# Performance work log

Hardware: AMD Instinct MI355X
Metric: run time of the kernel (lower is better)

Reference implementation:

```python
import jax, jax.numpy as jnp
import numpy as np

V, E, H, L, B, T = 8192, 64, 256, 2, 4, 512


def setup_inputs() -> dict:
    key = jax.random.key(0)
    ks = jax.random.split(key, 20)
    s = 0.02
    emb = (jax.random.normal(ks[0], (V, E)) * s).at[0].set(0.0)  # padding_idx=0
    x = jax.random.randint(ks[1], (B, T), 0, V)
    return {
        "x": x,
        "emb": emb,
        "W_ih0": jax.random.normal(ks[2], (H, E)) * s,
        "W_hh0": jax.random.normal(ks[3], (H, H)) * s,
        "b_ih0": jnp.zeros((H,), jnp.float32),
        "b_hh0": jnp.zeros((H,), jnp.float32),
        "W_ih1": jax.random.normal(ks[4], (H, H)) * s,
        "W_hh1": jax.random.normal(ks[5], (H, H)) * s,
        "b_ih1": jnp.zeros((H,), jnp.float32),
        "b_hh1": jnp.zeros((H,), jnp.float32),
        "Wq": jax.random.normal(ks[6], (H, H)) * s,
        "Wk": jax.random.normal(ks[7], (H, H)) * s,
        "v": jax.random.normal(ks[8], (H,)) * s,
        "gamma": jnp.ones((2 * H,), jnp.float32),
        "beta": jnp.zeros((2 * H,), jnp.float32),
        "Wfc": jax.random.normal(ks[9], (V, 2 * H)) * s,
        "bfc": jnp.zeros((V,), jnp.float32),
    }


def _rnn_layer(xs, W_ih, W_hh, b_ih, b_hh):
    # xs: (B, T, D) -> ys: (B, T, H), hT: (B, H). Vanilla tanh RNN.
    Bn = xs.shape[0]
    Hn = W_hh.shape[0]
    h0 = jnp.zeros((Bn, Hn), xs.dtype)

    def step(h, xt):
        h_new = jnp.tanh(xt @ W_ih.T + b_ih + h @ W_hh.T + b_hh)
        return h_new, h_new

    hT, ys = jax.lax.scan(step, h0, jnp.swapaxes(xs, 0, 1))
    return jnp.swapaxes(ys, 0, 1), hT


def reference(x, emb, W_ih0, W_hh0, b_ih0, b_hh0, W_ih1, W_hh1, b_ih1, b_hh1,
              Wq, Wk, v, gamma, beta, Wfc, bfc):
    # Dropout layers are identity (eval mode).
    e = emb[x]                                   # (B, T, E)
    y0, h0 = _rnn_layer(e, W_ih0, W_hh0, b_ih0, b_hh0)
    y1, h1 = _rnn_layer(y0, W_ih1, W_hh1, b_ih1, b_hh1)  # (B, T, H)

    # Bahdanau additive attention with causal mask
    q = y1 @ Wq.T                                # (B, T, H)
    k = y1 @ Wk.T                                # (B, T, H)
    # (B, Tq, Tk, H) broadcast add -> tanh -> contract with v
    scores = jnp.einsum('bijh,h->bij', jnp.tanh(q[:, :, None, :] + k[:, None, :, :]), v)
    Tn = scores.shape[1]
    causal = jnp.tril(jnp.ones((Tn, Tn), bool))
    scores = jnp.where(causal[None], scores, jnp.float32(-1e9))
    alpha = jax.nn.softmax(scores, axis=-1)      # (B, Tq, Tk)
    ctx = jnp.einsum('bij,bjh->bih', alpha, y1)  # bmm(alpha, K) with K = rnn_out

    cat = jnp.concatenate([y1, ctx], axis=-1)    # (B, T, 2H)
    mu = cat.mean(-1, keepdims=True)
    var = ((cat - mu) ** 2).mean(-1, keepdims=True)
    normed = (cat - mu) / jnp.sqrt(var + 1e-5) * gamma + beta

    logits = normed @ Wfc.T + bfc                # (B, T, V)
    h = jnp.stack([h0, h1], axis=0)              # (L, B, H)
    return logits, h
```

## Files before the change

kernel.cpp:

```cpp
#include <hip/hip_runtime.h>
#include <hip/hip_bf16.h>

typedef __bf16 bf16x8 __attribute__((ext_vector_type(8)));
typedef float  f32x4  __attribute__((ext_vector_type(4)));
typedef unsigned short u16;

#define T_N 512
#define H_N 256
#define B_N 4
#define V_N 8192
#define E_N 64

__device__ __forceinline__ float tanh_fast(float x) {
    float e = __expf(2.0f * x);
    return 1.0f - __fdividef(2.0f, e + 1.0f);
}

__device__ __forceinline__ float tanh_pade(float x) {
    x = fminf(3.0f, fmaxf(-3.0f, x));
    float x2 = x * x;
    float num = x * (945.0f + x2 * (105.0f + x2));
    float den = 945.0f + x2 * (420.0f + 15.0f * x2);
    return num * __frcp_rn(den);
}

__device__ __forceinline__ u16 f2bf(float f) {
    __hip_bfloat16 h = __float2bfloat16(f);
    return __builtin_bit_cast(u16, h);
}

__device__ __forceinline__ bf16x8 as_bf16x8(uint4 u) {
    return __builtin_bit_cast(bf16x8, u);
}

__device__ __forceinline__ uint4 pack_bf8(f32x4 lo, f32x4 hi) {
    union { u16 s[8]; uint4 u; } r;
    #pragma unroll
    for (int e = 0; e < 4; ++e) { r.s[e] = f2bf(lo[e]); r.s[e+4] = f2bf(hi[e]); }
    return r.u;
}

__device__ __forceinline__ f32x4 mfma16(bf16x8 a, bf16x8 b, f32x4 c) {
    return __builtin_amdgcn_mfma_f32_16x16x32_bf16(a, b, c, 0, 0, 0);
}

__global__ void cvt_bf16_kernel(const float* __restrict__ src, u16* __restrict__ dst, int n4) {
    int i = blockIdx.x * 256 + threadIdx.x;
    if (i < n4) {
        f32x4 v = ((const f32x4*)src)[i];
        union { u16 s[4]; unsigned long long u; } r;
        #pragma unroll
        for (int e = 0; e < 4; ++e) r.s[e] = f2bf(v[e]);
        ((unsigned long long*)dst)[i] = r.u;
    }
}

__global__ __launch_bounds__(256)
void prep_wih1_kernel(const float* __restrict__ Wih1, uint4* __restrict__ out) {
    const int f = blockIdx.x * 256 + threadIdx.x;
    const int jt = f >> 9, kk = (f >> 6) & 7, lo = f & 63;
    const int mo = lo & 15, go = lo >> 4;
    const float* p = Wih1 + (size_t)(jt * 16 + mo) * H_N + (kk << 5) + (go << 3);
    f32x4 a = *(const f32x4*)p;
    f32x4 b = *(const f32x4*)(p + 4);
    out[f] = pack_bf8(a, b);
}

__global__ __launch_bounds__(256)
void embed_xw0_kernel(const int* __restrict__ x, const float* __restrict__ emb,
                      const float* __restrict__ Wih, const float* __restrict__ bih,
                      const float* __restrict__ bhh, float* __restrict__ xw0) {
    const int t = blockIdx.x, tid = threadIdx.x;
    __shared__ float sE[4][64];
    {
        const int b = tid >> 6, k = tid & 63;
        sE[b][k] = emb[(size_t)x[b * T_N + t] * E_N + k];
    }
    __syncthreads();
    const int j = tid;
    const float* wr = Wih + j * E_N;
    float a0 = 0, a1 = 0, a2 = 0, a3 = 0;
    #pragma unroll 8
    for (int k = 0; k < E_N; ++k) {
        float wv = wr[k];
        a0 += sE[0][k] * wv; a1 += sE[1][k] * wv;
        a2 += sE[2][k] * wv; a3 += sE[3][k] * wv;
    }
    const float bs = bih[j] + bhh[j];
    f32x4 o = { a0 + bs, a1 + bs, a2 + bs, a3 + bs };
    *(f32x4*)(xw0 + ((size_t)t * H_N + j) * 4) = o;
}

__global__ __launch_bounds__(512, 2)
void rnn_fused_kernel(const float* __restrict__ Whh0, const float* __restrict__ Whh1,
                      const uint4* __restrict__ xfg, const float* __restrict__ bih1,
                      const float* __restrict__ bhh1, const float* __restrict__ xw0,
                      u16* __restrict__ y1bf, float* __restrict__ y1f,
                      float* __restrict__ hT) {
    __shared__ __align__(16) u16   ring[8][4][264];
    __shared__ __align__(16) u16   h1b[2][4][264];
    __shared__ __align__(16) float xwb[2][4][256][4];

    const int tid = threadIdx.x;
    const int w = tid >> 6, l = tid & 63;
    const int m = l & 15, g = l >> 4, b4 = m & 3;
    const int layer = w >> 2, wl = w & 3;
    const int jmy = (wl << 6) + l;

    for (int i = tid; i < 8 * 4 * 264; i += 512) (&ring[0][0][0])[i] = (u16)0;
    for (int i = tid; i < 2 * 4 * 264; i += 512) (&h1b[0][0][0])[i] = (u16)0;

    const float* Whh = (layer == 0) ? Whh0 : Whh1;
    bf16x8 wfrag[4][8];
    #pragma unroll
    for (int nt = 0; nt < 4; ++nt) {
        const int j = (wl << 6) + (nt << 4) + m;
        #pragma unroll
        for (int kk = 0; kk < 8; ++kk) {
            const float* p = Whh + (size_t)j * H_N + (kk << 5) + (g << 3);
            f32x4 lo4 = *(const f32x4*)p;
            f32x4 hi4 = *(const f32x4*)(p + 4);
            wfrag[nt][kk] = as_bf16x8(pack_bf8(lo4, hi4));
        }
    }

    const float bias1 = bih1[jmy] + bhh1[jmy];
    const f32x4* xwv = (const f32x4*)xw0;
    f32x4 xw_cur = xwv[jmy];
    const uint4* xgw = xfg + ((size_t)w << 10);

    __syncthreads();

    for (int it = 0; it < 517; ++it) {
        const bool burst = ((it & 3) == 0) && (it >= 4) && (it <= 512);

        uint4 xf0[8];
        if (burst) {
            #pragma unroll
            for (int kk = 0; kk < 8; ++kk) xf0[kk] = xgw[(kk << 6) + l];
        }

        if (layer == 0) {
            if (it < 512) {
                const int tn = (it + 1 < 512) ? it + 1 : it;
                f32x4 xw_nxt = xwv[(size_t)tn * H_N + jmy];
                const int rs = (it - 1) & 7;

                bf16x8 af[8];
                #pragma unroll
                for (int kk = 0; kk < 8; ++kk)
                    af[kk] = as_bf16x8(*(const uint4*)&ring[rs][b4][(kk << 5) + (g << 3)]);

                f32x4 ca[4], cb[4];
                #pragma unroll
                for (int nt = 0; nt < 4; ++nt) {
                    ca[nt] = (f32x4){0.f, 0.f, 0.f, 0.f};
                    cb[nt] = (f32x4){0.f, 0.f, 0.f, 0.f};
                }
                #pragma unroll
                for (int kk = 0; kk < 4; ++kk)
                    #pragma unroll
                    for (int nt = 0; nt < 4; ++nt) {
                        ca[nt] = mfma16(af[kk],     wfrag[nt][kk],     ca[nt]);
                        cb[nt] = mfma16(af[kk + 4], wfrag[nt][kk + 4], cb[nt]);
                    }

                f32x4 hv = (g == 0) ? (ca[0] + cb[0])
                         : (g == 1) ? (ca[1] + cb[1])
                         : (g == 2) ? (ca[2] + cb[2])
                         :            (ca[3] + cb[3]);
                hv += xw_cur;

                #pragma unroll
                for (int b = 0; b < 4; ++b) {
                    float hn = tanh_fast(hv[b]);
                    ring[it & 7][b][jmy] = f2bf(hn);
                    if (it == T_N - 1) hT[b * H_N + jmy] = hn;
                }
                xw_cur = xw_nxt;
            }
        } else {
            if (it >= 5) {
                const int s = it - 5;
                f32x4 xws = *(const f32x4*)&xwb[(s >> 2) & 1][s & 3][jmy][0];
                const int rs = (s - 1) & 1;

                bf16x8 af[8];
                #pragma unroll
                for (int kk = 0; kk < 8; ++kk)
                    af[kk] = as_bf16x8(*(const uint4*)&h1b[rs][b4][(kk << 5) + (g << 3)]);

                f32x4 ca[4], cb[4];
                #pragma unroll
                for (int nt = 0; nt < 4; ++nt) {
                    ca[nt] = (f32x4){0.f, 0.f, 0.f, 0.f};
                    cb[nt] = (f32x4){0.f, 0.f, 0.f, 0.f};
                }
                #pragma unroll
                for (int kk = 0; kk < 4; ++kk)
                    #pragma unroll
                    for (int nt = 0; nt < 4; ++nt) {
                        ca[nt] = mfma16(af[kk],     wfrag[nt][kk],     ca[nt]);
                        cb[nt] = mfma16(af[kk + 4], wfrag[nt][kk + 4], cb[nt]);
                    }

                f32x4 hv = (g == 0) ? (ca[0] + cb[0])
                         : (g == 1) ? (ca[1] + cb[1])
                         : (g == 2) ? (ca[2] + cb[2])
                         :            (ca[3] + cb[3]);
                hv += xws;
                hv += (f32x4){bias1, bias1, bias1, bias1};

                #pragma unroll
                for (int b = 0; b < 4; ++b) {
                    float hn = tanh_fast(hv[b]);
                    u16 bits = f2bf(hn);
                    h1b[s & 1][b][jmy] = bits;
                    y1bf[((size_t)b * T_N + s) * H_N + jmy] = bits;
                    y1f [((size_t)b * T_N + s) * H_N + jmy] = hn;
                    if (s == T_N - 1) hT[1024 + b * H_N + jmy] = hn;
                }
            }
        }

        if (burst) {
            const int t0 = it - 4;
            const int par = ((it - 4) >> 2) & 1;
            const int slotm = (t0 + (m >> 2)) & 7;
            bf16x8 ax[8];
            #pragma unroll
            for (int kk = 0; kk < 8; ++kk)
                ax[kk] = as_bf16x8(*(const uint4*)&ring[slotm][b4][(kk << 5) + (g << 3)]);

            f32x4 xa0 = {0.f, 0.f, 0.f, 0.f};
            #pragma unroll
            for (int kk = 0; kk < 8; ++kk)
                xa0 = mfma16(ax[kk], as_bf16x8(xf0[kk]), xa0);

            uint4 xf1[8];
            #pragma unroll
            for (int kk = 0; kk < 8; ++kk) xf1[kk] = xgw[512 + (kk << 6) + l];

            f32x4 xa1 = {0.f, 0.f, 0.f, 0.f};
            #pragma unroll
            for (int kk = 0; kk < 8; ++kk)
                xa1 = mfma16(ax[kk], as_bf16x8(xf1[kk]), xa1);

            *(f32x4*)&xwb[par][g][(w << 5) + m][0]      = xa0;
            *(f32x4*)&xwb[par][g][(w << 5) + 16 + m][0] = xa1;
        }

        asm volatile("s_waitcnt lgkmcnt(0)\n\ts_barrier" ::: "memory");
    }
}

template<int MODE>
__global__ __launch_bounds__(256, 2)
void gemm_bf16(const u16* __restrict__ A, const u16* __restrict__ Bw,
               float* __restrict__ out, const float* __restrict__ bias,
               const float* __restrict__ bias2, int M, int N, int K) {
    __shared__ __align__(16) u16 As[64][40];
    __shared__ __align__(16) u16 Bs[64][40];
    const int tid = threadIdx.x;
    const int nb = N >> 6;
    const int bm = blockIdx.x / nb, bn = blockIdx.x % nb;
    const int l = tid & 63, w = tid >> 6;
    const int wm = w & 1, wn = w >> 1;
    const int m = l & 15, g = l >> 4;
    const int srow = tid >> 2, sseg = tid & 3;

    f32x4 c[2][2];
    #pragma unroll
    for (int i = 0; i < 2; ++i)
        #pragma unroll
        for (int j = 0; j < 2; ++j) c[i][j] = (f32x4){0.f, 0.f, 0.f, 0.f};

    const u16* ap = A  + (size_t)(bm * 64 + srow) * K + sseg * 8;
    const u16* bp = Bw + (size_t)(bn * 64 + srow) * K + sseg * 8;

    for (int k0 = 0; k0 < K; k0 += 32) {
        uint4 av = *(const uint4*)(ap + k0);
        uint4 bv = *(const uint4*)(bp + k0);
        __syncthreads();
        *(uint4*)&As[srow][sseg << 3] = av;
        *(uint4*)&Bs[srow][sseg << 3] = bv;
        __syncthreads();
        bf16x8 af[2], bfr[2];
        #pragma unroll
        for (int i = 0; i < 2; ++i) {
            af[i]  = as_bf16x8(*(const uint4*)&As[(wm << 5) + (i << 4) + m][g << 3]);
            bfr[i] = as_bf16x8(*(const uint4*)&Bs[(wn << 5) + (i << 4) + m][g << 3]);
        }
        #pragma unroll
        for (int i = 0; i < 2; ++i)
            #pragma unroll
            for (int j = 0; j < 2; ++j)
                c[i][j] = mfma16(af[i], bfr[j], c[i][j]);
    }

    #pragma unroll
    for (int i = 0; i < 2; ++i)
        #pragma unroll
        for (int j = 0; j < 2; ++j) {
            const int col = (bn << 6) + (wn << 5) + (j << 4) + m;
            float bs = 0.f;
            if (bias)  bs += bias[col];
            if (bias2) bs += bias2[col];
            #pragma unroll
            for (int r = 0; r < 4; ++r) {
                const int row = (bm << 6) + (wm << 5) + (i << 4) + (g << 2) + r;
                const float val = c[i][j][r] + bs;
                if (MODE == 0) {
                    out[(size_t)row * N + col] = val;
                } else {
                    const int b = row >> 9, t = row & 511;
                    out[(size_t)b * N * T_N + (size_t)col * T_N + t] = val;
                }
            }
        }
}

__global__ __launch_bounds__(256, 2)
void gemm_fc(const u16* __restrict__ A, const u16* __restrict__ Bw,
             const float* __restrict__ bias, float* __restrict__ out) {
    __shared__ __align__(16) u16 As[128 * 32];
    __shared__ __align__(16) u16 Bs[128 * 32];
    const int tid = threadIdx.x;
    const int l = tid & 63, w = tid >> 6;
    const int m = l & 15, g = l >> 4;
    const int wm = w >> 1, wn = w & 1;
    const int bm = blockIdx.x >> 6, bn = blockIdx.x & 63;
    constexpr int K = 512;

    f32x4 acc[4][4];
    #pragma unroll
    for (int i = 0; i < 4; ++i)
        #pragma unroll
        for (int j = 0; j < 4; ++j) acc[i][j] = (f32x4){0.f, 0.f, 0.f, 0.f};

    const u16* aBase = A  + (size_t)(bm * 128) * K;
    const u16* bBase = Bw + (size_t)(bn * 128) * K;
    const int row0 = tid >> 2,          seg0 = tid & 3;
    const int row1 = (tid + 256) >> 2,  seg1 = tid & 3;
    const int wseg0 = seg0 ^ ((row0 >> 1) & 3);
    const int wseg1 = seg1 ^ ((row1 >> 1) & 3);

    for (int k0 = 0; k0 < K; k0 += 32) {
        uint4 av0 = *(const uint4*)(aBase + (size_t)row0 * K + k0 + seg0 * 8);
        uint4 av1 = *(const uint4*)(aBase + (size_t)row1 * K + k0 + seg1 * 8);
        uint4 bv0 = *(const uint4*)(bBase + (size_t)row0 * K + k0 + seg0 * 8);
        uint4 bv1 = *(const uint4*)(bBase + (size_t)row1 * K + k0 + seg1 * 8);
        __syncthreads();
        *(uint4*)((char*)As + row0 * 64 + wseg0 * 16) = av0;
        *(uint4*)((char*)As + row1 * 64 + wseg1 * 16) = av1;
        *(uint4*)((char*)Bs + row0 * 64 + wseg0 * 16) = bv0;
        *(uint4*)((char*)Bs + row1 * 64 + wseg1 * 16) = bv1;
        __syncthreads();
        bf16x8 af[4], bfr[4];
        #pragma unroll
        for (int i = 0; i < 4; ++i) {
            const int arow = wm * 64 + i * 16 + m;
            const int aslot = g ^ ((arow >> 1) & 3);
            af[i]  = as_bf16x8(*(const uint4*)((char*)As + arow * 64 + aslot * 16));
            const int brow = wn * 64 + i * 16 + m;
            const int bslot = g ^ ((brow >> 1) & 3);
            bfr[i] = as_bf16x8(*(const uint4*)((char*)Bs + brow * 64 + bslot * 16));
        }
        #pragma unroll
        for (int i = 0; i < 4; ++i)
            #pragma unroll
            for (int j = 0; j < 4; ++j)
                acc[i][j] = mfma16(af[i], bfr[j], acc[i][j]);
    }

    #pragma unroll
    for (int i = 0; i < 4; ++i)
        #pragma unroll
        for (int j = 0; j < 4; ++j) {
            const int col = bn * 128 + wn * 64 + j * 16 + m;
            const float bs = bias[col];
            #pragma unroll
            for (int r = 0; r < 4; ++r) {
                const int row = bm * 128 + wm * 64 + i * 16 + (g << 2) + r;
                out[(size_t)row * V_N + col] = acc[i][j][r] + bs;
            }
        }
}

__global__ __launch_bounds__(256)
void attn_kernel(const float* __restrict__ q, const float* __restrict__ kT,
                 const float* __restrict__ y1f, const float* __restrict__ vvec,
                 float* __restrict__ ctx) {
    const int blk = blockIdx.x;
    const int b = blk >> 9, i = blk & 511;
    const int tid = threadIdx.x;
    __shared__ float sQ[H_N], sV[H_N], sS[T_N];
    __shared__ float red[4];
    sQ[tid] = q[((size_t)b * T_N + i) * H_N + tid];
    sV[tid] = vvec[tid];
    __syncthreads();

    float s0 = -1e30f, s1 = -1e30f;
    if (tid <= i) {
        const float* kp = kT + (size_t)b * H_N * T_N + tid;
        float acc = 0.f;
        for (int h = 0; h < H_N; ++h) acc += sV[h] * tanh_pade(sQ[h] + kp[(size_t)h * T_N]);
        s0 = acc;
    }
    if (tid + 256 <= i) {
        const float* kp = kT + (size_t)b * H_N * T_N + tid + 256;
        float acc = 0.f;
        for (int h = 0; h < H_N; ++h) acc += sV[h] * tanh_pade(sQ[h] + kp[(size_t)h * T_N]);
        s1 = acc;
    }
    float mv = fmaxf(s0, s1);
    #pragma unroll
    for (int o = 32; o; o >>= 1) mv = fmaxf(mv, __shfl_xor(mv, o, 64));
    if ((tid & 63) == 0) red[tid >> 6] = mv;
    __syncthreads();
    mv = fmaxf(fmaxf(red[0], red[1]), fmaxf(red[2], red[3]));
    __syncthreads();
    float e0 = (tid <= i)       ? __expf(s0 - mv) : 0.f;
    float e1 = (tid + 256 <= i) ? __expf(s1 - mv) : 0.f;
    float sm = e0 + e1;
    #pragma unroll
    for (int o = 32; o; o >>= 1) sm += __shfl_xor(sm, o, 64);
    if ((tid & 63) == 0) red[tid >> 6] = sm;
    __syncthreads();
    sm = red[0] + red[1] + red[2] + red[3];
    const float rs = 1.0f / sm;
    sS[tid] = e0 * rs;
    sS[tid + 256] = e1 * rs;
    __syncthreads();
    float acc = 0.f;
    const float* yp = y1f + (size_t)b * T_N * H_N + tid;
    for (int j2 = 0; j2 <= i; ++j2) acc += sS[j2] * yp[(size_t)j2 * H_N];
    ctx[((size_t)b * T_N + i) * H_N + tid] = acc;
}

__global__ __launch_bounds__(256)
void ln_kernel(const float* __restrict__ y1f, const float* __restrict__ ctx,
               const float* __restrict__ gamma, const float* __restrict__ beta,
               u16* __restrict__ outbf) {
    const int row = blockIdx.x, tid = threadIdx.x;
    __shared__ float red[4];
    const float x1 = y1f[(size_t)row * H_N + tid];
    const float x2 = ctx[(size_t)row * H_N + tid];
    float s = x1 + x2;
    #pragma unroll
    for (int o = 32; o; o >>= 1) s += __shfl_xor(s, o, 64);
    if ((tid & 63) == 0) red[tid >> 6] = s;
    __syncthreads();
    const float mu = (red[0] + red[1] + red[2] + red[3]) * (1.f / 512.f);
    __syncthreads();
    const float d1 = x1 - mu, d2 = x2 - mu;
    float qv = d1 * d1 + d2 * d2;
    #pragma unroll
    for (int o = 32; o; o >>= 1) qv += __shfl_xor(qv, o, 64);
    if ((tid & 63) == 0) red[tid >> 6] = qv;
    __syncthreads();
    const float var = (red[0] + red[1] + red[2] + red[3]) * (1.f / 512.f);
    const float inv = rsqrtf(var + 1e-5f);
    outbf[(size_t)row * 512 + tid]       = f2bf(d1 * inv * gamma[tid] + beta[tid]);
    outbf[(size_t)row * 512 + tid + 256] = f2bf(d2 * inv * gamma[tid + 256] + beta[tid + 256]);
}

extern "C" void kernel_launch(void* const* d_in, const int* in_sizes, int n_in,
                              void* d_out, int out_size, void* d_ws, size_t ws_size,
                              hipStream_t stream) {
    const int*   x     = (const int*)  d_in[0];
    const float* emb   = (const float*)d_in[1];
    const float* Wih0  = (const float*)d_in[2];
    const float* Whh0  = (const float*)d_in[3];
    const float* bih0  = (const float*)d_in[4];
    const float* bhh0  = (const float*)d_in[5];
    const float* Wih1  = (const float*)d_in[6];
    const float* Whh1  = (const float*)d_in[7];
    const float* bih1  = (const float*)d_in[8];
    const float* bhh1  = (const float*)d_in[9];
    const float* Wq    = (const float*)d_in[10];
    const float* Wk    = (const float*)d_in[11];
    const float* vvec  = (const float*)d_in[12];
    const float* gamma = (const float*)d_in[13];
    const float* beta  = (const float*)d_in[14];
    const float* Wfc   = (const float*)d_in[15];
    const float* bfc   = (const float*)d_in[16];

    float* outp = (float*)d_out;
    char* ws = (char*)d_ws;
    float* xw0   = (float*)(ws + 0);
    uint4* xfg   = (uint4*)(ws + 2097152);
    u16*   y1bf  = (u16*)  (ws + 5242880);
    float* y1f   = (float*)(ws + 6291456);
    float* qf    = (float*)(ws + 8388608);
    float* kT    = (float*)(ws + 10485760);
    float* ctx   = (float*)(ws + 12582912);
    u16*   nrm   = (u16*)  (ws + 14680064);
    u16*   Wqb   = (u16*)  (ws + 16908288);
    u16*   Wkb   = (u16*)  (ws + 17039360);
    u16*   Wfcb  = (u16*)  (ws + 17170432);

    float* hout = outp + (size_t)B_N * T_N * V_N;

    cvt_bf16_kernel<<<64,   256, 0, stream>>>(Wq,  Wqb,  65536 / 4);
    cvt_bf16_kernel<<<64,   256, 0, stream>>>(Wk,  Wkb,  65536 / 4);
    cvt_bf16_kernel<<<4096, 256, 0, stream>>>(Wfc, Wfcb, 4194304 / 4);
    prep_wih1_kernel<<<32, 256, 0, stream>>>(Wih1, xfg);

    embed_xw0_kernel<<<512, 256, 0, stream>>>(x, emb, Wih0, bih0, bhh0, xw0);
    rnn_fused_kernel<<<1, 512, 0, stream>>>(Whh0, Whh1, xfg, bih1, bhh1,
                                            xw0, y1bf, y1f, hout);
    gemm_bf16<0><<<32 * 4, 256, 0, stream>>>(y1bf, Wqb, qf, nullptr, nullptr, 2048, 256, 256);
    gemm_bf16<2><<<32 * 4, 256, 0, stream>>>(y1bf, Wkb, kT, nullptr, nullptr, 2048, 256, 256);
    attn_kernel<<<2048, 256, 0, stream>>>(qf, kT, y1f, vvec, ctx);
    ln_kernel<<<2048, 256, 0, stream>>>(y1f, ctx, gamma, beta, nrm);
    gemm_fc<<<16 * 64, 256, 0, stream>>>(nrm, Wfcb, bfc, outp);
}
```

Measured before the change: 876.5 us.

## Split fused RNN recurrence across 16 waves instead of 8

The single-block fused two-layer RNN kernel goes from 512 to 1024 threads. Each wave now owns 32 hidden units instead of 64, which halves the per-step MFMA chain and the weight registers per wave. The layer-1 input projection burst is repartitioned per wave, with the bias folded in and xwb transposed and padded. Half the lanes in each wave sit idle during the tanh/store phase, and the wider block pays more barrier cost per step.

```diff
diff --git a/kernel.cpp b/kernel.cpp
--- a/kernel.cpp
+++ b/kernel.cpp
@@ -91,30 +91,31 @@
     *(f32x4*)(xw0 + ((size_t)t * H_N + j) * 4) = o;
 }
 
-__global__ __launch_bounds__(512, 2)
-void rnn_fused_kernel(const float* __restrict__ Whh0, const float* __restrict__ Whh1,
-                      const uint4* __restrict__ xfg, const float* __restrict__ bih1,
-                      const float* __restrict__ bhh1, const float* __restrict__ xw0,
-                      u16* __restrict__ y1bf, float* __restrict__ y1f,
-                      float* __restrict__ hT) {
+__global__ __launch_bounds__(1024)
+void rnn_fused16_kernel(const float* __restrict__ Whh0, const float* __restrict__ Whh1,
+                        const uint4* __restrict__ xfg, const float* __restrict__ bih1,
+                        const float* __restrict__ bhh1, const float* __restrict__ xw0,
+                        u16* __restrict__ y1bf, float* __restrict__ y1f,
+                        float* __restrict__ hT) {
     __shared__ __align__(16) u16   ring[8][4][264];
     __shared__ __align__(16) u16   h1b[2][4][264];
-    __shared__ __align__(16) float xwb[2][4][256][4];
+    __shared__ __align__(16) float xwb[2][4][4][265];
 
     const int tid = threadIdx.x;
     const int w = tid >> 6, l = tid & 63;
     const int m = l & 15, g = l >> 4, b4 = m & 3;
-    const int layer = w >> 2, wl = w & 3;
-    const int jmy = (wl << 6) + l;
-
-    for (int i = tid; i < 8 * 4 * 264; i += 512) (&ring[0][0][0])[i] = (u16)0;
-    for (int i = tid; i < 2 * 4 * 264; i += 512) (&h1b[0][0][0])[i] = (u16)0;
+    const int layer = w >> 3, wl = w & 7;
+    const bool act = (g < 2);
+    const int jmy = (wl << 5) + ((g & 1) << 4) + m;
+
+    for (int i = tid; i < 8 * 4 * 264; i += 1024) (&ring[0][0][0])[i] = (u16)0;
+    for (int i = tid; i < 2 * 4 * 264; i += 1024) (&h1b[0][0][0])[i] = (u16)0;
 
     const float* Whh = (layer == 0) ? Whh0 : Whh1;
-    bf16x8 wfrag[4][8];
-    #pragma unroll
-    for (int nt = 0; nt < 4; ++nt) {
-        const int j = (wl << 6) + (nt << 4) + m;
+    bf16x8 wfrag[2][8];
+    #pragma unroll
+    for (int nt = 0; nt < 2; ++nt) {
+        const int j = (wl << 5) + (nt << 4) + m;
         #pragma unroll
         for (int kk = 0; kk < 8; ++kk) {
             const float* p = Whh + (size_t)j * H_N + (kk << 5) + (g << 3);
@@ -124,21 +125,16 @@
         }
     }
 
-    const float bias1 = bih1[jmy] + bhh1[jmy];
+    const int jb = (w << 4) + m;
+    const float biasb = bih1[jb] + bhh1[jb];
+
     const f32x4* xwv = (const f32x4*)xw0;
     f32x4 xw_cur = xwv[jmy];
-    const uint4* xgw = xfg + ((size_t)w << 10);
 
     __syncthreads();
 
     for (int it = 0; it < 517; ++it) {
         const bool burst = ((it & 3) == 0) && (it >= 4) && (it <= 512);
-
-        uint4 xf0[8];
-        if (burst) {
-            #pragma unroll
-            for (int kk = 0; kk < 8; ++kk) xf0[kk] = xgw[(kk << 6) + l];
-        }
 
         if (layer == 0) {
             if (it < 512) {
@@ -151,38 +147,31 @@
                 for (int kk = 0; kk < 8; ++kk)
                     af[kk] = as_bf16x8(*(const uint4*)&ring[rs][b4][(kk << 5) + (g << 3)]);
 
-                f32x4 ca[4], cb[4];
+                f32x4 c0 = {0.f, 0.f, 0.f, 0.f}, c1 = {0.f, 0.f, 0.f, 0.f};
                 #pragma unroll
-                for (int nt = 0; nt < 4; ++nt) {
-                    ca[nt] = (f32x4){0.f, 0.f, 0.f, 0.f};
-                    cb[nt] = (f32x4){0.f, 0.f, 0.f, 0.f};
+                for (int kk = 0; kk < 8; ++kk) {
+                    c0 = mfma16(af[kk], wfrag[0][kk], c0);
+                    c1 = mfma16(af[kk], wfrag[1][kk], c1);
                 }
-                #pragma unroll
-                for (int kk = 0; kk < 4; ++kk)
+                f32x4 hv = (g & 1) ? c1 : c0;
+                hv += xw_cur;
+
+                if (act) {
                     #pragma unroll
-                    for (int nt = 0; nt < 4; ++nt) {
-                        ca[nt] = mfma16(af[kk],     wfrag[nt][kk],     ca[nt]);
-                        cb[nt] = mfma16(af[kk + 4], wfrag[nt][kk + 4], cb[nt]);
+                    for (int b = 0; b < 4; ++b) {
+                        float hn = tanh_fast(hv[b]);
+                        ring[it & 7][b][jmy] = f2bf(hn);
+                        if (it == T_N - 1) hT[b * H_N + jmy] = hn;
                     }
-
-                f32x4 hv = (g == 0) ? (ca[0] + cb[0])
-                         : (g == 1) ? (ca[1] + cb[1])
-                         : (g == 2) ? (ca[2] + cb[2])
-                         :            (ca[3] + cb[3]);
-                hv += xw_cur;
-
-                #pragma unroll
-                for (int b = 0; b < 4; ++b) {
-                    float hn = tanh_fast(hv[b]);
-                    ring[it & 7][b][jmy] = f2bf(hn);
-                    if (it == T_N - 1) hT[b * H_N + jmy] = hn;
                 }
                 xw_cur = xw_nxt;
             }
         } else {
             if (it >= 5) {
                 const int s = it - 5;
-                f32x4 xws = *(const f32x4*)&xwb[(s >> 2) & 1][s & 3][jmy][0];
+                const int par = (s >> 2) & 1, d = s & 3;
+                f32x4 xws = { xwb[par][d][0][jmy], xwb[par][d][1][jmy],
+                              xwb[par][d][2][jmy], xwb[par][d][3][jmy] };
                 const int rs = (s - 1) & 1;
 
                 bf16x8 af[8];
@@ -190,35 +179,25 @@
                 for (int kk = 0; kk < 8; ++kk)
                     af[kk] = as_bf16x8(*(const uint4*)&h1b[rs][b4][(kk << 5) + (g << 3)]);
 
-                f32x4 ca[4], cb[4];
+                f32x4 c0 = {0.f, 0.f, 0.f, 0.f}, c1 = {0.f, 0.f, 0.f, 0.f};
                 #pragma unroll
-                for (int nt = 0; nt < 4; ++nt) {
-                    ca[nt] = (f32x4){0.f, 0.f, 0.f, 0.f};
-                    cb[nt] = (f32x4){0.f, 0.f, 0.f, 0.f};
+                for (int kk = 0; kk < 8; ++kk) {
+                    c0 = mfma16(af[kk], wfrag[0][kk], c0);
+                    c1 = mfma16(af[kk], wfrag[1][kk], c1);
                 }
-                #pragma unroll
-                for (int kk = 0; kk < 4; ++kk)
+                f32x4 hv = (g & 1) ? c1 : c0;
+                hv += xws;
+
+                if (act) {
                     #pragma unroll
-                    for (int nt = 0; nt < 4; ++nt) {
-                        ca[nt] = mfma16(af[kk],     wfrag[nt][kk],     ca[nt]);
-                        cb[nt] = mfma16(af[kk + 4], wfrag[nt][kk + 4], cb[nt]);
+                    for (int b = 0; b < 4; ++b) {
+                        float hn = tanh_fast(hv[b]);
+                        u16 bits = f2bf(hn);
+                        h1b[s & 1][b][jmy] = bits;
+                        y1bf[((size_t)b * T_N + s) * H_N + jmy] = bits;
+                        y1f [((size_t)b * T_N + s) * H_N + jmy] = hn;
+                        if (s == T_N - 1) hT[1024 + b * H_N + jmy] = hn;
                     }
-
-                f32x4 hv = (g == 0) ? (ca[0] + cb[0])
-                         : (g == 1) ? (ca[1] + cb[1])
-                         : (g == 2) ? (ca[2] + cb[2])
-                         :            (ca[3] + cb[3]);
-                hv += xws;
-                hv += (f32x4){bias1, bias1, bias1, bias1};
-
-                #pragma unroll
-                for (int b = 0; b < 4; ++b) {
-                    float hn = tanh_fast(hv[b]);
-                    u16 bits = f2bf(hn);
-                    h1b[s & 1][b][jmy] = bits;
-                    y1bf[((size_t)b * T_N + s) * H_N + jmy] = bits;
-                    y1f [((size_t)b * T_N + s) * H_N + jmy] = hn;
-                    if (s == T_N - 1) hT[1024 + b * H_N + jmy] = hn;
                 }
             }
         }
@@ -232,22 +211,24 @@
             for (int kk = 0; kk < 8; ++kk)
                 ax[kk] = as_bf16x8(*(const uint4*)&ring[slotm][b4][(kk << 5) + (g << 3)]);
 
-            f32x4 xa0 = {0.f, 0.f, 0.f, 0.f};
-            #pragma unroll
-            for (int kk = 0; kk < 8; ++kk)
-                xa0 = mfma16(ax[kk], as_bf16x8(xf0[kk]), xa0);
-
-            uint4 xf1[8];
-            #pragma unroll
-            for (int kk = 0; kk < 8; ++kk) xf1[kk] = xgw[512 + (kk << 6) + l];
-
-            f32x4 xa1 = {0.f, 0.f, 0.f, 0.f};
-            #pragma unroll
-            for (int kk = 0; kk < 8; ++kk)
-                xa1 = mfma16(ax[kk], as_bf16x8(xf1[kk]), xa1);
-
-            *(f32x4*)&xwb[par][g][(w << 5) + m][0]      = xa0;
-            *(f32x4*)&xwb[par][g][(w << 5) + 16 + m][0] = xa1;
+            uint4 xf0[4];
+            #pragma unroll
+            for (int kk = 0; kk < 4; ++kk) xf0[kk] = xfg[((w << 3) + kk) * 64 + l];
+            f32x4 xa = {0.f, 0.f, 0.f, 0.f};
+            #pragma unroll
+            for (int kk = 0; kk < 4; ++kk) xa = mfma16(ax[kk], as_bf16x8(xf0[kk]), xa);
+
+            uint4 xf1[4];
+            #pragma unroll
+            for (int kk = 0; kk < 4; ++kk) xf1[kk] = xfg[((w << 3) + 4 + kk) * 64 + l];
+            f32x4 ya = {0.f, 0.f, 0.f, 0.f};
+            #pragma unroll
+            for (int kk = 0; kk < 4; ++kk) ya = mfma16(ax[kk + 4], as_bf16x8(xf1[kk]), ya);
+            xa += ya;
+
+            #pragma unroll
+            for (int r = 0; r < 4; ++r)
+                xwb[par][g][r][jb] = xa[r] + biasb;
         }
 
         asm volatile("s_waitcnt lgkmcnt(0)\n\ts_barrier" ::: "memory");
@@ -508,8 +489,8 @@
     prep_wih1_kernel<<<32, 256, 0, stream>>>(Wih1, xfg);
 
     embed_xw0_kernel<<<512, 256, 0, stream>>>(x, emb, Wih0, bih0, bhh0, xw0);
-    rnn_fused_kernel<<<1, 512, 0, stream>>>(Whh0, Whh1, xfg, bih1, bhh1,
-                                            xw0, y1bf, y1f, hout);
+    rnn_fused16_kernel<<<1, 1024, 0, stream>>>(Whh0, Whh1, xfg, bih1, bhh1,
+                                               xw0, y1bf, y1f, hout);
     gemm_bf16<0><<<32 * 4, 256, 0, stream>>>(y1bf, Wqb, qf, nullptr, nullptr, 2048, 256, 256);
     gemm_bf16<2><<<32 * 4, 256, 0, stream>>>(y1bf, Wkb, kT, nullptr, nullptr, 2048, 256, 256);
     attn_kernel<<<2048, 256, 0, stream>>>(qf, kT, y1f, vvec, ctx);
```

New measurement: 910.2 us. 1.04x slower.
